# Kernel optimization log

Measured on AMD Instinct MI355X. Metric: run time of the kernel, lower is better.

The kernel has to match this reference:

```python
import jax, jax.numpy as jnp
import numpy as np
from jax import lax

STRIDE = 2  # down_sample_stride
MATMUL_NORM = True


def maxpool2d_5d(x, s):
    # x: [B, T, C, H, W]; kernel=s, stride=s, padding=(s-1)//2 == 0 for s=2
    return lax.reduce_window(
        x, -jnp.inf, lax.max,
        window_dimensions=(1, 1, 1, s, s),
        window_strides=(1, 1, 1, s, s),
        padding='VALID')


def setup_inputs() -> dict:
    key = jax.random.key(0)
    k1, k2, k3, k4 = jax.random.split(key, 4)
    B, T, Ck, Cv, H, W = 2, 4, 64, 256, 64, 64
    return {
        'memory_keys': jax.random.normal(k1, (B, T, Ck, H, W), jnp.float32),
        'memory_values': jax.random.normal(k2, (B, T, Cv, H, W), jnp.float32),
        'query_key': jax.random.normal(k3, (B, Ck, H, W), jnp.float32),
        'query_value': jax.random.normal(k4, (B, Cv, H, W), jnp.float32),
    }


def reference(memory_keys, memory_values, query_key, query_value):
    B, T, Ck, oH, oW = memory_keys.shape
    Cv = memory_values.shape[2]
    # down-sample memory bank (max pool, stride 2, no padding)
    mk = maxpool2d_5d(memory_keys, STRIDE)   # [B,T,Ck,h,w]
    mv = maxpool2d_5d(memory_values, STRIDE) # [B,T,Cv,h,w]
    h, w = mk.shape[-2], mk.shape[-1]
    M = T * h * w
    N = oH * oH  # code uses ori_height*ori_height (square assumed)
    # permute(0,2,1,3,4).view(B,Ck,M).permute(0,2,1) -> [B, M, Ck]
    mk = mk.transpose(0, 2, 1, 3, 4).reshape(B, Ck, M).transpose(0, 2, 1)
    qk = query_key.reshape(B, Ck, N)
    attn = jnp.einsum('bmc,bcn->bmn', mk, qk)  # [B, M, N]
    if MATMUL_NORM:
        attn = attn * (Ck ** -0.5)
    attn = jax.nn.softmax(attn, axis=1)  # softmax over memory positions
    mv = mv.transpose(0, 2, 1, 3, 4).reshape(B, Cv, M)
    memory = jnp.einsum('bcm,bmn->bcn', mv, attn).reshape(B, Cv, oH, oW)
    return jnp.concatenate([query_value, memory], axis=1)  # [B, 2*Cv, H, W]
```

## Files before the change

### kernel.cpp

```cpp
#include <hip/hip_runtime.h>
#include <hip/hip_bf16.h>

typedef unsigned short u16;
typedef unsigned int   u32;
typedef __attribute__((ext_vector_type(8))) short  bf16x8;
typedef __attribute__((ext_vector_type(4))) float  floatx4;

#define NB 2
#define NT 4
#define CK 64
#define CV 256
#define HH 64
#define WW 64
#define MM 4096
#define NN 4096
#define SCALE 0.125f
#define SHIFT 4.0f
#define OUT_B 2097152
#define MSPLIT 2
#define MHALF 2048
#define ITERS 32

__device__ __forceinline__ u16 f2b(float f) {
    __hip_bfloat16 h = __float2bfloat16(f);
    union { __hip_bfloat16 h; u16 u; } v; v.h = h; return v.u;
}


__global__ void pool_k_bf(const float* __restrict__ src, u16* __restrict__ dst) {
    int e = blockIdx.x * 256 + threadIdx.x;
    int m = e & 4095; int c = (e >> 12) & 63; int b = e >> 18;
    int ww = m & 31, hh = (m >> 5) & 31, t = m >> 10;
    const float* s = src + ((size_t)(((b*NT + t)*CK + c)*HH + 2*hh))*WW + 2*ww;
    dst[((size_t)b*MM + m)*CK + c] = f2b(fmaxf(fmaxf(s[0], s[1]), fmaxf(s[WW], s[WW+1])));
}

__global__ void pool_v_bf(const float* __restrict__ src, u16* __restrict__ dst) {
    int e = blockIdx.x * 256 + threadIdx.x;
    int m = e & 4095; int c = (e >> 12) & 255; int b = e >> 20;
    int ww = m & 31, hh = (m >> 5) & 31, t = m >> 10;
    const float* s = src + ((size_t)(((b*NT + t)*CV + c)*HH + 2*hh))*WW + 2*ww;
    dst[((size_t)b*CV + c)*MM + m] = f2b(fmaxf(fmaxf(s[0], s[1]), fmaxf(s[WW], s[WW+1])));
}

__global__ void copy_qv(const float4* __restrict__ src, float4* __restrict__ dst) {
    int u = blockIdx.x * 256 + threadIdx.x;
    int b  = u >> 18;
    int ru = u & 262143;
    dst[(size_t)b * (OUT_B/4) + ru] = src[u];
}

__launch_bounds__(256)
__global__ void attn_mfma(const u16* __restrict__ pk, const u16* __restrict__ vt,
                          const float* __restrict__ qk,
                          float* __restrict__ part, float* __restrict__ sums) {
    const int ntile = blockIdx.x, b = blockIdx.y, ms = blockIdx.z;
    const int tid = threadIdx.x, w = tid >> 6, l = tid & 63;
    const int lrow = l & 15, quad = l >> 4;
    const int n0 = ntile * 64;
    const int m0 = ms * MHALF;

    __shared__ u16  P_lds[64][72];
    __shared__ float sums_s[4][64];

    bf16x8 qf[2][4];
    const float* qb = qk + (size_t)b * CK * NN;
    #pragma unroll
    for (int cc = 0; cc < 2; ++cc)
        #pragma unroll
        for (int t = 0; t < 4; ++t) {
            int n = n0 + t*16 + lrow;
            #pragma unroll
            for (int i = 0; i < 8; ++i) {
                int c = cc*32 + quad*8 + i;
                qf[cc][t][i] = (short)f2b(qb[(size_t)c*NN + n]);
            }
        }

    const u16* pkb = pk + (size_t)b * MM * CK;
    const u16* vtb = vt + (size_t)b * CV * MM;

    floatx4 oacc[4][4];
    #pragma unroll
    for (int j = 0; j < 4; ++j)
        #pragma unroll
        for (int t = 0; t < 4; ++t)
            oacc[j][t] = (floatx4){0.f, 0.f, 0.f, 0.f};
    float sacc[4] = {0.f, 0.f, 0.f, 0.f};

    for (int it = 0; it < ITERS; ++it) {
        const int mbase = m0 + it * 64;

        const u16* kp = pkb + (size_t)(mbase + w*16 + lrow)*CK + quad*8;
        bf16x8 kf0 = *(const bf16x8*)(kp);
        bf16x8 kf1 = *(const bf16x8*)(kp + 32);

        bf16x8 vf[2][4];
        #pragma unroll
        for (int j = 0; j < 4; ++j) {
            const u16* vp = vtb + (size_t)(w*64 + j*16 + lrow)*MM + mbase + quad*8;
            vf[0][j] = *(const bf16x8*)(vp);
            vf[1][j] = *(const bf16x8*)(vp + 32);
        }

        #pragma unroll
        for (int t = 0; t < 4; ++t) {
            floatx4 s = __builtin_amdgcn_mfma_f32_16x16x32_bf16(
                            kf0, qf[0][t], (floatx4){0.f,0.f,0.f,0.f}, 0, 0, 0);
            s = __builtin_amdgcn_mfma_f32_16x16x32_bf16(kf1, qf[1][t], s, 0, 0, 0);
            float p0 = __expf(s[0]*SCALE - SHIFT);
            float p1 = __expf(s[1]*SCALE - SHIFT);
            float p2 = __expf(s[2]*SCALE - SHIFT);
            float p3 = __expf(s[3]*SCALE - SHIFT);
            sacc[t] += (p0 + p1) + (p2 + p3);
            u32 d0 = (u32)f2b(p0) | ((u32)f2b(p1) << 16);
            u32 d1 = (u32)f2b(p2) | ((u32)f2b(p3) << 16);
            uint2* pdst = (uint2*)&P_lds[t*16 + lrow][w*16 + quad*4];
            *pdst = make_uint2(d0, d1);
        }
        __syncthreads();

        #pragma unroll
        for (int cc = 0; cc < 2; ++cc) {
            bf16x8 pf[4];
            #pragma unroll
            for (int t = 0; t < 4; ++t)
                pf[t] = *(const bf16x8*)&P_lds[t*16 + lrow][cc*32 + quad*8];
            #pragma unroll
            for (int j = 0; j < 4; ++j)
                #pragma unroll
                for (int t = 0; t < 4; ++t)
                    oacc[j][t] = __builtin_amdgcn_mfma_f32_16x16x32_bf16(
                                     vf[cc][j], pf[t], oacc[j][t], 0, 0, 0);
        }
        __syncthreads();
    }

    #pragma unroll
    for (int t = 0; t < 4; ++t) {
        float v = sacc[t];
        v += __shfl_xor(v, 16, 64);
        v += __shfl_xor(v, 32, 64);
        if (l < 16) sums_s[w][t*16 + l] = v;
    }
    __syncthreads();

    float* pb = part + ((size_t)((ms*NB + b)*64 + ntile)) * (256*64);
    #pragma unroll
    for (int j = 0; j < 4; ++j)
        #pragma unroll
        for (int t = 0; t < 4; ++t)
            #pragma unroll
            for (int r = 0; r < 4; ++r) {
                int c = w*64 + j*16 + quad*4 + r;
                int n = t*16 + lrow;
                pb[c*64 + n] = oacc[j][t][r];
            }
    if (tid < 64) {
        float sv = sums_s[0][tid] + sums_s[1][tid] + sums_s[2][tid] + sums_s[3][tid];
        sums[((size_t)((ms*NB + b)*64 + ntile))*64 + tid] = sv;
    }
}

__global__ void attn_reduce(const float* __restrict__ part, const float* __restrict__ sums,
                            float* __restrict__ out) {
    int e = blockIdx.x * 256 + threadIdx.x;
    int n = e & 4095;
    int c = (e >> 12) & 255;
    int b = e >> 20;
    int ntile = n >> 6, nl = n & 63;
    size_t t0 = ((size_t)((0*NB + b)*64 + ntile));
    size_t t1 = ((size_t)((1*NB + b)*64 + ntile));
    float num = part[t0*16384 + c*64 + nl] + part[t1*16384 + c*64 + nl];
    float den = sums[t0*64 + nl] + sums[t1*64 + nl];
    out[((size_t)(b*512 + 256 + c))*NN + n] = num / den;
}


__global__ void pool_v_f32(const float* __restrict__ src, float* __restrict__ out) {
    int e = blockIdx.x * 256 + threadIdx.x;
    int c = e & 255;
    int r = e >> 8;
    int ww = r & 31;  int hh = (r >> 5) & 31;
    int t  = (r >> 10) & 3;  int b = r >> 12;
    int m  = r & (MM - 1);
    const float* s = src + ((size_t)(((b*NT + t)*CV + c)*HH + 2*hh))*WW + 2*ww;
    out[(size_t)b*OUT_B + (size_t)m*CV + c] = fmaxf(fmaxf(s[0], s[1]), fmaxf(s[WW], s[WW+1]));
}

__global__ void pool_k_f32(const float* __restrict__ src, float* __restrict__ dst) {
    int e = blockIdx.x * 256 + threadIdx.x;
    int c = e & 63;
    int r = e >> 6;
    int ww = r & 31;  int hh = (r >> 5) & 31;
    int t  = (r >> 10) & 3;  int b = r >> 12;
    const float* s = src + ((size_t)(((b*NT + t)*CK + c)*HH + 2*hh))*WW + 2*ww;
    dst[e] = fmaxf(fmaxf(s[0], s[1]), fmaxf(s[WW], s[WW+1]));
}

template<bool STAGED_K>
__launch_bounds__(256)
__global__ void attn_old(const float* __restrict__ pk,
                         const float* __restrict__ mk,
                         const float* __restrict__ qk,
                         float* __restrict__ out) {
    __shared__ __align__(16) float q_lds[CK][4];
    __shared__ __align__(16) float sarr[4][MM];
    __shared__ float inv_l[4];

    const int tid = threadIdx.x;
    const int blk = blockIdx.x;
    const int b   = blk >> 10;
    const int n0  = (blk & 1023) << 2;

    {
        int c = tid >> 2, qi = tid & 3;
        q_lds[c][qi] = qk[((size_t)(b*CK + c))*NN + n0 + qi];
    }
    __syncthreads();

    #pragma unroll
    for (int i = 0; i < 16; ++i) {
        int m = tid + (i << 8);
        float a0 = 0.f, a1 = 0.f, a2 = 0.f, a3 = 0.f;
        if (STAGED_K) {
            const float4* k4 = reinterpret_cast<const float4*>(pk + ((size_t)b*MM + m)*CK);
            #pragma unroll
            for (int cc = 0; cc < 16; ++cc) {
                float4 kv = k4[cc];
                int c = cc*4;
                float4 q0 = *reinterpret_cast<const float4*>(&q_lds[c][0]);
                float4 q1 = *reinterpret_cast<const float4*>(&q_lds[c+1][0]);
                float4 q2 = *reinterpret_cast<const float4*>(&q_lds[c+2][0]);
                float4 q3 = *reinterpret_cast<const float4*>(&q_lds[c+3][0]);
                a0 += kv.x*q0.x + kv.y*q1.x + kv.z*q2.x + kv.w*q3.x;
                a1 += kv.x*q0.y + kv.y*q1.y + kv.z*q2.y + kv.w*q3.y;
                a2 += kv.x*q0.z + kv.y*q1.z + kv.z*q2.z + kv.w*q3.z;
                a3 += kv.x*q0.w + kv.y*q1.w + kv.z*q2.w + kv.w*q3.w;
            }
        } else {
            int ww = m & 31, hh = (m >> 5) & 31, t = m >> 10;
            const float* base = mk + ((size_t)((b*NT + t)*CK)*HH + 2*hh)*WW + 2*ww;
            for (int c = 0; c < CK; ++c) {
                const float* s = base + (size_t)c*HH*WW;
                float kv = fmaxf(fmaxf(s[0], s[1]), fmaxf(s[WW], s[WW+1]));
                float4 q = *reinterpret_cast<const float4*>(&q_lds[c][0]);
                a0 += kv*q.x; a1 += kv*q.y; a2 += kv*q.z; a3 += kv*q.w;
            }
        }
        sarr[0][m] = a0*SCALE;
        sarr[1][m] = a1*SCALE;
        sarr[2][m] = a2*SCALE;
        sarr[3][m] = a3*SCALE;
    }
    __syncthreads();

    const int wave = tid >> 6, lane = tid & 63;
    float mx = -3.0e38f;
    for (int m = lane; m < MM; m += 64) mx = fmaxf(mx, sarr[wave][m]);
    #pragma unroll
    for (int off = 32; off > 0; off >>= 1) mx = fmaxf(mx, __shfl_xor(mx, off, 64));
    float ls = 0.f;
    for (int m = lane; m < MM; m += 64) {
        float p = __expf(sarr[wave][m] - mx);
        sarr[wave][m] = p;
        ls += p;
    }
    #pragma unroll
    for (int off = 32; off > 0; off >>= 1) ls += __shfl_xor(ls, off, 64);
    if (lane == 0) inv_l[wave] = 1.0f / ls;
    __syncthreads();

    const int c4 = lane;
    const float4* vb = reinterpret_cast<const float4*>(out + (size_t)b*OUT_B) + c4;
    const float* prow = sarr[wave];
    float a0 = 0.f, a1 = 0.f, a2 = 0.f, a3 = 0.f;
    for (int m = 0; m < MM; m += 4) {
        float4 p4 = *reinterpret_cast<const float4*>(prow + m);
        const float4* vp = vb + (size_t)m*(CV/4);
        float4 v0 = vp[0], v1 = vp[CV/4], v2 = vp[CV/2], v3 = vp[3*(CV/4)];
        a0 += p4.x*v0.x + p4.y*v1.x + p4.z*v2.x + p4.w*v3.x;
        a1 += p4.x*v0.y + p4.y*v1.y + p4.z*v2.y + p4.w*v3.y;
        a2 += p4.x*v0.z + p4.y*v1.z + p4.z*v2.z + p4.w*v3.z;
        a3 += p4.x*v0.w + p4.y*v1.w + p4.z*v2.w + p4.w*v3.w;
    }

    float inv = inv_l[wave];
    int n = n0 + wave;
    size_t ob = ((size_t)(b*512 + 256 + c4*4))*NN + n;
    out[ob]        = a0*inv;
    out[ob + NN]   = a1*inv;
    out[ob + 2*NN] = a2*inv;
    out[ob + 3*NN] = a3*inv;
}


extern "C" void kernel_launch(void* const* d_in, const int* in_sizes, int n_in,
                              void* d_out, int out_size, void* d_ws, size_t ws_size,
                              hipStream_t stream) {
    const float* mk = (const float*)d_in[0];
    const float* mv = (const float*)d_in[1];
    const float* qk = (const float*)d_in[2];
    const float* qv = (const float*)d_in[3];
    float* out = (float*)d_out;

    u16* pk_bf = (u16*)d_ws;
    u16* vt_bf = pk_bf + (size_t)NB*MM*CK;
    float* part = (float*)(vt_bf + (size_t)NB*CV*MM);
    float* sums = part + (size_t)MSPLIT*NB*64*256*64 / 256;
    sums = part + 4194304;
    const size_t need = (size_t)NB*MM*CK*2 + (size_t)NB*CV*MM*2
                      + (4194304 + 16384) * sizeof(float);

    if (ws_size >= need) {
        pool_k_bf<<<(NB*MM*CK)/256, 256, 0, stream>>>(mk, pk_bf);
        pool_v_bf<<<(NB*MM*CV)/256, 256, 0, stream>>>(mv, vt_bf);
        attn_mfma<<<dim3(64, NB, MSPLIT), 256, 0, stream>>>(pk_bf, vt_bf, qk, part, sums);
        attn_reduce<<<(NB*CV*NN)/256, 256, 0, stream>>>(part, sums, out);
        copy_qv<<<((NB*CV*HH*WW)/4)/256, 256, 0, stream>>>((const float4*)qv, (float4*)out);
    } else {
        const size_t pk_bytes = (size_t)NB*MM*CK*sizeof(float);
        const bool staged = (ws_size >= pk_bytes);
        float* pk = (float*)d_ws;
        pool_v_f32<<<(NB*MM*CV)/256, 256, 0, stream>>>(mv, out);
        if (staged) {
            pool_k_f32<<<(NB*MM*CK)/256, 256, 0, stream>>>(mk, pk);
            attn_old<true ><<<NB*(NN/4), 256, 0, stream>>>(pk, mk, qk, out);
        } else {
            attn_old<false><<<NB*(NN/4), 256, 0, stream>>>(pk, mk, qk, out);
        }
        copy_qv<<<((NB*CV*HH*WW)/4)/256, 256, 0, stream>>>((const float4*)qv, (float4*)out);
    }
}
```

Baseline: 155.6 us.

## Fuse pooling kernels, widen attention block to 8 waves, fuse epilogue with copy

Merges the two pooling kernels into one launch and folds the query-value copy into a vectorized float4 reduction epilogue, cutting five launches to three. The attention kernel now runs 512 threads with 8 waves, each covering 128 memory positions per iteration and 32 value channels, which halves the iteration count. The P tile in LDS is XOR-swizzled to avoid bank conflicts. The cost is fewer output accumulators per wave and more LDS traffic per output element, plus a larger block that may lower occupancy.

Result: faster. 148.2 us (-4.8%).

```diff
diff --git a/kernel.cpp b/kernel.cpp
--- a/kernel.cpp
+++ b/kernel.cpp
@@ -19,7 +19,7 @@
 #define OUT_B 2097152
 #define MSPLIT 2
 #define MHALF 2048
-#define ITERS 32
+#define ITERS 16
 
 __device__ __forceinline__ u16 f2b(float f) {
     __hip_bfloat16 h = __float2bfloat16(f);
@@ -27,30 +27,27 @@
 }
 
 
-__global__ void pool_k_bf(const float* __restrict__ src, u16* __restrict__ dst) {
+#define KTOT (NB*MM*CK)
+__global__ void pool_kv(const float* __restrict__ mk, const float* __restrict__ mv,
+                        u16* __restrict__ pk, u16* __restrict__ vt) {
     int e = blockIdx.x * 256 + threadIdx.x;
-    int m = e & 4095; int c = (e >> 12) & 63; int b = e >> 18;
-    int ww = m & 31, hh = (m >> 5) & 31, t = m >> 10;
-    const float* s = src + ((size_t)(((b*NT + t)*CK + c)*HH + 2*hh))*WW + 2*ww;
-    dst[((size_t)b*MM + m)*CK + c] = f2b(fmaxf(fmaxf(s[0], s[1]), fmaxf(s[WW], s[WW+1])));
-}
-
-__global__ void pool_v_bf(const float* __restrict__ src, u16* __restrict__ dst) {
-    int e = blockIdx.x * 256 + threadIdx.x;
-    int m = e & 4095; int c = (e >> 12) & 255; int b = e >> 20;
-    int ww = m & 31, hh = (m >> 5) & 31, t = m >> 10;
-    const float* s = src + ((size_t)(((b*NT + t)*CV + c)*HH + 2*hh))*WW + 2*ww;
-    dst[((size_t)b*CV + c)*MM + m] = f2b(fmaxf(fmaxf(s[0], s[1]), fmaxf(s[WW], s[WW+1])));
-}
-
-__global__ void copy_qv(const float4* __restrict__ src, float4* __restrict__ dst) {
-    int u = blockIdx.x * 256 + threadIdx.x;
-    int b  = u >> 18;
-    int ru = u & 262143;
-    dst[(size_t)b * (OUT_B/4) + ru] = src[u];
-}
-
-__launch_bounds__(256)
+    if (e < KTOT) {
+        int m = e & 4095; int c = (e >> 12) & 63; int b = e >> 18;
+        int ww = m & 31, hh = (m >> 5) & 31, t = m >> 10;
+        const float* s = mk + ((size_t)(((b*NT + t)*CK + c)*HH + 2*hh))*WW + 2*ww;
+        pk[((size_t)b*MM + m)*CK + c] =
+            f2b(fmaxf(fmaxf(s[0], s[1]), fmaxf(s[WW], s[WW+1])));
+    } else {
+        int e2 = e - KTOT;
+        int m = e2 & 4095; int c = (e2 >> 12) & 255; int b = e2 >> 20;
+        int ww = m & 31, hh = (m >> 5) & 31, t = m >> 10;
+        const float* s = mv + ((size_t)(((b*NT + t)*CV + c)*HH + 2*hh))*WW + 2*ww;
+        vt[((size_t)b*CV + c)*MM + m] =
+            f2b(fmaxf(fmaxf(s[0], s[1]), fmaxf(s[WW], s[WW+1])));
+    }
+}
+
+__launch_bounds__(512)
 __global__ void attn_mfma(const u16* __restrict__ pk, const u16* __restrict__ vt,
                           const float* __restrict__ qk,
                           float* __restrict__ part, float* __restrict__ sums) {
@@ -60,8 +57,8 @@
     const int n0 = ntile * 64;
     const int m0 = ms * MHALF;
 
-    __shared__ u16  P_lds[64][72];
-    __shared__ float sums_s[4][64];
+    __shared__ u16  P[64 * 128];
+    __shared__ float sums_s[8][64];
 
     bf16x8 qf[2][4];
     const float* qb = qk + (size_t)b * CK * NN;
@@ -80,27 +77,31 @@
     const u16* pkb = pk + (size_t)b * MM * CK;
     const u16* vtb = vt + (size_t)b * CV * MM;
 
-    floatx4 oacc[4][4];
-    #pragma unroll
-    for (int j = 0; j < 4; ++j)
+    floatx4 oacc[2][4];
+    #pragma unroll
+    for (int j = 0; j < 2; ++j)
         #pragma unroll
         for (int t = 0; t < 4; ++t)
             oacc[j][t] = (floatx4){0.f, 0.f, 0.f, 0.f};
     float sacc[4] = {0.f, 0.f, 0.f, 0.f};
 
+    const int sw = lrow << 1;
+
     for (int it = 0; it < ITERS; ++it) {
-        const int mbase = m0 + it * 64;
+        const int mbase = m0 + it * 128;
 
         const u16* kp = pkb + (size_t)(mbase + w*16 + lrow)*CK + quad*8;
         bf16x8 kf0 = *(const bf16x8*)(kp);
         bf16x8 kf1 = *(const bf16x8*)(kp + 32);
 
-        bf16x8 vf[2][4];
-        #pragma unroll
-        for (int j = 0; j < 4; ++j) {
-            const u16* vp = vtb + (size_t)(w*64 + j*16 + lrow)*MM + mbase + quad*8;
+        bf16x8 vf[4][2];
+        #pragma unroll
+        for (int j = 0; j < 2; ++j) {
+            const u16* vp = vtb + (size_t)(w*32 + j*16 + lrow)*MM + mbase + quad*8;
             vf[0][j] = *(const bf16x8*)(vp);
             vf[1][j] = *(const bf16x8*)(vp + 32);
+            vf[2][j] = *(const bf16x8*)(vp + 64);
+            vf[3][j] = *(const bf16x8*)(vp + 96);
         }
 
         #pragma unroll
@@ -115,19 +116,23 @@
             sacc[t] += (p0 + p1) + (p2 + p3);
             u32 d0 = (u32)f2b(p0) | ((u32)f2b(p1) << 16);
             u32 d1 = (u32)f2b(p2) | ((u32)f2b(p3) << 16);
-            uint2* pdst = (uint2*)&P_lds[t*16 + lrow][w*16 + quad*4];
-            *pdst = make_uint2(d0, d1);
+            int n_l = t*16 + lrow;
+            int cb  = (w << 2) + quad;
+            *(uint2*)&P[n_l*128 + ((cb ^ sw) << 2)] = make_uint2(d0, d1);
         }
         __syncthreads();
 
         #pragma unroll
-        for (int cc = 0; cc < 2; ++cc) {
+        for (int cc = 0; cc < 4; ++cc) {
             bf16x8 pf[4];
             #pragma unroll
-            for (int t = 0; t < 4; ++t)
-                pf[t] = *(const bf16x8*)&P_lds[t*16 + lrow][cc*32 + quad*8];
-            #pragma unroll
-            for (int j = 0; j < 4; ++j)
+            for (int t = 0; t < 4; ++t) {
+                int n_l = t*16 + lrow;
+                int cb  = (cc << 3) + (quad << 1);
+                pf[t] = *(const bf16x8*)&P[n_l*128 + ((cb ^ sw) << 2)];
+            }
+            #pragma unroll
+            for (int j = 0; j < 2; ++j)
                 #pragma unroll
                 for (int t = 0; t < 4; ++t)
                     oacc[j][t] = __builtin_amdgcn_mfma_f32_16x16x32_bf16(
@@ -147,33 +152,50 @@
 
     float* pb = part + ((size_t)((ms*NB + b)*64 + ntile)) * (256*64);
     #pragma unroll
-    for (int j = 0; j < 4; ++j)
+    for (int j = 0; j < 2; ++j)
         #pragma unroll
         for (int t = 0; t < 4; ++t)
             #pragma unroll
             for (int r = 0; r < 4; ++r) {
-                int c = w*64 + j*16 + quad*4 + r;
+                int c = w*32 + j*16 + quad*4 + r;
                 int n = t*16 + lrow;
                 pb[c*64 + n] = oacc[j][t][r];
             }
     if (tid < 64) {
-        float sv = sums_s[0][tid] + sums_s[1][tid] + sums_s[2][tid] + sums_s[3][tid];
+        float sv = 0.f;
+        #pragma unroll
+        for (int ww2 = 0; ww2 < 8; ++ww2) sv += sums_s[ww2][tid];
         sums[((size_t)((ms*NB + b)*64 + ntile))*64 + tid] = sv;
     }
 }
 
-__global__ void attn_reduce(const float* __restrict__ part, const float* __restrict__ sums,
-                            float* __restrict__ out) {
+__global__ void epilogue(const float* __restrict__ part, const float* __restrict__ sums,
+                         const float4* __restrict__ qv, float* __restrict__ out) {
     int e = blockIdx.x * 256 + threadIdx.x;
-    int n = e & 4095;
-    int c = (e >> 12) & 255;
-    int b = e >> 20;
-    int ntile = n >> 6, nl = n & 63;
-    size_t t0 = ((size_t)((0*NB + b)*64 + ntile));
-    size_t t1 = ((size_t)((1*NB + b)*64 + ntile));
-    float num = part[t0*16384 + c*64 + nl] + part[t1*16384 + c*64 + nl];
-    float den = sums[t0*64 + nl] + sums[t1*64 + nl];
-    out[((size_t)(b*512 + 256 + c))*NN + n] = num / den;
+    if (e < 524288) {
+        int b = e >> 18; int ru = e & 262143;
+        ((float4*)out)[(size_t)b*(OUT_B/4) + ru] = qv[e];
+    } else {
+        int e4 = e - 524288;
+        int nl4   = e4 & 15;
+        int ntile = (e4 >> 4) & 63;
+        int c     = (e4 >> 10) & 255;
+        int b     = e4 >> 18;
+        size_t t0 = (size_t)(0*NB + b)*64 + ntile;
+        size_t t1 = (size_t)(1*NB + b)*64 + ntile;
+        const float4* p4 = (const float4*)part;
+        const float4* s4 = (const float4*)sums;
+        float4 u0 = p4[t0*4096 + c*16 + nl4];
+        float4 u1 = p4[t1*4096 + c*16 + nl4];
+        float4 d0 = s4[t0*16 + nl4];
+        float4 d1 = s4[t1*16 + nl4];
+        float4 r;
+        r.x = (u0.x + u1.x) / (d0.x + d1.x);
+        r.y = (u0.y + u1.y) / (d0.y + d1.y);
+        r.z = (u0.z + u1.z) / (d0.z + d1.z);
+        r.w = (u0.w + u1.w) / (d0.w + d1.w);
+        ((float4*)out)[(size_t)(b*512 + 256 + c)*1024 + ntile*16 + nl4] = r;
+    }
 }
 
 
@@ -196,6 +218,13 @@
     int t  = (r >> 10) & 3;  int b = r >> 12;
     const float* s = src + ((size_t)(((b*NT + t)*CK + c)*HH + 2*hh))*WW + 2*ww;
     dst[e] = fmaxf(fmaxf(s[0], s[1]), fmaxf(s[WW], s[WW+1]));
+}
+
+__global__ void copy_qv_f32(const float4* __restrict__ src, float4* __restrict__ dst) {
+    int u = blockIdx.x * 256 + threadIdx.x;
+    int b  = u >> 18;
+    int ru = u & 262143;
+    dst[(size_t)b * (OUT_B/4) + ru] = src[u];
 }
 
 template<bool STAGED_K>
@@ -307,17 +336,14 @@
     u16* pk_bf = (u16*)d_ws;
     u16* vt_bf = pk_bf + (size_t)NB*MM*CK;
     float* part = (float*)(vt_bf + (size_t)NB*CV*MM);
-    float* sums = part + (size_t)MSPLIT*NB*64*256*64 / 256;
-    sums = part + 4194304;
+    float* sums = part + 4194304;
     const size_t need = (size_t)NB*MM*CK*2 + (size_t)NB*CV*MM*2
                       + (4194304 + 16384) * sizeof(float);
 
     if (ws_size >= need) {
-        pool_k_bf<<<(NB*MM*CK)/256, 256, 0, stream>>>(mk, pk_bf);
-        pool_v_bf<<<(NB*MM*CV)/256, 256, 0, stream>>>(mv, vt_bf);
-        attn_mfma<<<dim3(64, NB, MSPLIT), 256, 0, stream>>>(pk_bf, vt_bf, qk, part, sums);
-        attn_reduce<<<(NB*CV*NN)/256, 256, 0, stream>>>(part, sums, out);
-        copy_qv<<<((NB*CV*HH*WW)/4)/256, 256, 0, stream>>>((const float4*)qv, (float4*)out);
+        pool_kv<<<(KTOT + NB*MM*CV)/256, 256, 0, stream>>>(mk, mv, pk_bf, vt_bf);
+        attn_mfma<<<dim3(64, NB, MSPLIT), 512, 0, stream>>>(pk_bf, vt_bf, qk, part, sums);
+        epilogue<<<(2*524288)/256, 256, 0, stream>>>(part, sums, (const float4*)qv, out);
     } else {
         const size_t pk_bytes = (size_t)NB*MM*CK*sizeof(float);
         const bool staged = (ws_size >= pk_bytes);
@@ -329,6 +355,6 @@
         } else {
             attn_old<false><<<NB*(NN/4), 256, 0, stream>>>(pk, mk, qk, out);
         }
-        copy_qv<<<((NB*CV*HH*WW)/4)/256, 256, 0, stream>>>((const float4*)qv, (float4*)out);
-    }
-}
+        copy_qv_f32<<<((NB*CV*HH*WW)/4)/256, 256, 0, stream>>>((const float4*)qv, (float4*)out);
+    }
+}
```
